# Optimization experiments

Hardware: AMD Instinct MI355X
Metric: run time of the kernel (lower is better)

Reference implementation:

```python
import jax, jax.numpy as jnp
import numpy as np

EPS = 1e-6


def setup_inputs() -> dict:
    key = jax.random.key(0)
    k1, _ = jax.random.split(key)
    L, D = 128, 262144
    slots = jax.random.normal(k1, (L, D), dtype=jnp.float32)
    temperature = jnp.ones((), dtype=jnp.float32)  # temperature = 1.0
    return {"slots": slots, "temperature": temperature, "length": L}


def reference(slots, temperature, length):
    # slots: [L, D]; pairwise cosine similarity (torch: x.y / max(|x||y|, eps))
    L = length
    norms = jnp.sqrt(jnp.sum(slots * slots, axis=1))                # [L]
    gram = jnp.einsum('id,jd->ij', slots, slots)                    # [L, L]
    sim = gram / jnp.maximum(norms[:, None] * norms[None, :], EPS)  # [L, L]
    logits = sim / temperature
    E = jnp.exp(logits)                                             # [L, L]
    # denominator for pair (i, j): sum_{k != j} exp(sim(i,k)/T)  (k=i included)
    denom = jnp.sum(E, axis=1, keepdims=True) - E                   # [L, L]
    log_ratio = logits - jnp.log(denom)                             # log(num/den)
    idx = jnp.arange(L)
    penalty = jnp.abs(idx[:, None] - idx[None, :]).astype(slots.dtype)  # |i-j|
    upper = (idx[:, None] < idx[None, :]).astype(slots.dtype)           # i < j
    total = jnp.sum(-log_ratio * penalty * upper)
    # original divides by i*j/2 with final loop values i=j=length-1
    total = total / ((L - 1) * (L - 1) / 2.0)
    return total
```

## Files before the change

### kernel.cpp

```cpp
#include <hip/hip_runtime.h>
#include <hip/hip_bf16.h>

typedef __attribute__((ext_vector_type(8))) short bf16x8;
typedef __attribute__((ext_vector_type(4))) float f32x4;

constexpr int L  = 128;
constexpr int BK = 128;
constexpr int LDS_PITCH = BK * 2;
constexpr int GRID = 512;

__device__ inline bf16x8 ld_frag(const char* lds, int row, int kk, int lane) {
    int byteoff = row * LDS_PITCH + (kk + 8 * (lane >> 4)) * 2;
    byteoff ^= (row & 7) << 4;
    return *reinterpret_cast<const bf16x8*>(lds + byteoff);
}

__global__ __launch_bounds__(256, 2)
void gram_kernel(const float* __restrict__ slots, float* __restrict__ partial,
                 int D, int nChunks, int G) {
    __shared__ __align__(16) char lds[2][L * LDS_PITCH];
    const int t    = threadIdx.x;
    const int wave = t >> 6;
    const int lane = t & 63;

    f32x4 acc[2][8];
#pragma unroll
    for (int r = 0; r < 2; ++r)
#pragma unroll
        for (int c = 0; c < 8; ++c) acc[r][c] = (f32x4)0.f;

    float4 ld[16];

    auto issue = [&](int chunk) {
        const size_t c0 = (size_t)chunk * BK;
#pragma unroll
        for (int q = 0; q < 16; ++q) {
            int idx  = t + 256 * q;
            int row  = idx >> 5;
            int col4 = idx & 31;
            ld[q] = *reinterpret_cast<const float4*>(
                slots + (size_t)row * D + c0 + (size_t)col4 * 4);
        }
    };
    auto commit = [&](int buf) {
#pragma unroll
        for (int q = 0; q < 16; ++q) {
            int idx  = t + 256 * q;
            int row  = idx >> 5;
            int col4 = idx & 31;
            const unsigned int* f = reinterpret_cast<const unsigned int*>(&ld[q]);
            uint2 p;
            p.x = __builtin_amdgcn_perm(f[1], f[0], 0x07060302u);
            p.y = __builtin_amdgcn_perm(f[3], f[2], 0x07060302u);
            int byteoff = row * LDS_PITCH + col4 * 8;
            byteoff ^= (row & 7) << 4;
            *reinterpret_cast<uint2*>(&lds[buf][0] + byteoff) = p;
        }
    };

    issue(blockIdx.x);
    commit(0);
    __syncthreads();

    int k = 0;
    for (int c = blockIdx.x; c < nChunks; c += G, ++k) {
        const int nxt = c + G;
        if (nxt < nChunks) issue(nxt);
        const int cur = k & 1;

#pragma unroll
        for (int kk = 0; kk < BK; kk += 32) {
            bf16x8 a0 = ld_frag(&lds[cur][0], wave * 32 +      (lane & 15), kk, lane);
            bf16x8 a1 = ld_frag(&lds[cur][0], wave * 32 + 16 + (lane & 15), kk, lane);
#pragma unroll
            for (int cc = 0; cc < 8; ++cc) {
                bf16x8 b = ld_frag(&lds[cur][0], cc * 16 + (lane & 15), kk, lane);
                acc[0][cc] = __builtin_amdgcn_mfma_f32_16x16x32_bf16(a0, b, acc[0][cc], 0, 0, 0);
                acc[1][cc] = __builtin_amdgcn_mfma_f32_16x16x32_bf16(a1, b, acc[1][cc], 0, 0, 0);
            }
        }

        if (nxt < nChunks) commit(cur ^ 1);
        __syncthreads();
    }

    float* pb = partial + (size_t)blockIdx.x * (L * L);
#pragma unroll
    for (int r = 0; r < 2; ++r)
#pragma unroll
        for (int c = 0; c < 8; ++c)
            *reinterpret_cast<float4*>(pb + (r * 8 + c) * 1024 + t * 4) =
                *reinterpret_cast<float4*>(&acc[r][c]);
}

__global__ void zero_kernel(float* __restrict__ p, int n) {
    int i = blockIdx.x * 256 + threadIdx.x;
    if (i < n) p[i] = 0.f;
}

__global__ void reduce_kernel(const float* __restrict__ partial, float* __restrict__ gram,
                              int G, int span) {
    const int id = blockIdx.x * 256 + threadIdx.x;
    const int b0 = blockIdx.y * span;
    const int b1 = (b0 + span < G) ? b0 + span : G;

    float4 sum = make_float4(0.f, 0.f, 0.f, 0.f);
    for (int b = b0; b < b1; ++b) {
        const float4 v = *reinterpret_cast<const float4*>(
            partial + (size_t)b * (L * L) + (size_t)id * 4);
        sum.x += v.x; sum.y += v.y; sum.z += v.z; sum.w += v.w;
    }
    const int tt   = id & 255;
    const int slot = id >> 8;
    const int wave = tt >> 6, lane = tt & 63;
    const int r = slot >> 3, c = slot & 7;
    const int growb = wave * 32 + r * 16 + ((lane >> 4) << 2);
    const int gcol  = c * 16 + (lane & 15);
    atomicAdd(&gram[(growb + 0) * L + gcol], sum.x);
    atomicAdd(&gram[(growb + 1) * L + gcol], sum.y);
    atomicAdd(&gram[(growb + 2) * L + gcol], sum.z);
    atomicAdd(&gram[(growb + 3) * L + gcol], sum.w);
}

__global__ __launch_bounds__(1024, 1)
void finalize_kernel(const float* __restrict__ gram,
                     const float* __restrict__ temperature,
                     float* __restrict__ out) {
    __shared__ float g[L * L];
    __shared__ float norms[L];
    __shared__ float wsum[16];
    const int t = threadIdx.x;

#pragma unroll
    for (int q = 0; q < 4; ++q) {
        int i = t + 1024 * q;
        *reinterpret_cast<float4*>(&g[i * 4]) =
            *reinterpret_cast<const float4*>(&gram[i * 4]);
    }
    __syncthreads();
    if (t < L) norms[t] = sqrtf(g[t * L + t]);
    __syncthreads();

    const float invT = 1.0f / temperature[0];
    const int r = t >> 3;
    const int q = t & 7;
    const float ni = norms[r];

    float ps = 0.f;
    for (int j = q; j < L; j += 8) {
        float sim = g[r * L + j] / fmaxf(ni * norms[j], 1e-6f);
        ps += __expf(sim * invT);
    }
    ps += __shfl_xor(ps, 1);
    ps += __shfl_xor(ps, 2);
    ps += __shfl_xor(ps, 4);
    const float rowsum = ps;

    float tot = 0.f;
    for (int j = q; j < L; j += 8) {
        if (j > r) {
            float logit = (g[r * L + j] / fmaxf(ni * norms[j], 1e-6f)) * invT;
            float e = __expf(logit);
            tot += -(logit - __logf(rowsum - e)) * (float)(j - r);
        }
    }
#pragma unroll
    for (int s = 1; s < 64; s <<= 1) tot += __shfl_xor(tot, s);
    if ((t & 63) == 0) wsum[t >> 6] = tot;
    __syncthreads();
    if (t == 0) {
        float s = 0.f;
        for (int w = 0; w < 16; ++w) s += wsum[w];
        out[0] = s / ((float)(L - 1) * (float)(L - 1) * 0.5f);
    }
}

extern "C" void kernel_launch(void* const* d_in, const int* in_sizes, int n_in,
                              void* d_out, int out_size, void* d_ws, size_t ws_size,
                              hipStream_t stream) {
    const float* slots       = (const float*)d_in[0];
    const float* temperature = (const float*)d_in[1];
    float* out  = (float*)d_out;

    const int D = in_sizes[0] / L;
    const int nChunks = D / BK;
    int G = GRID;
    if (G > nChunks) G = nChunks;

    float* partial = (float*)d_ws;
    float* gram    = (float*)d_ws + (size_t)G * L * L;

    zero_kernel<<<(L * L + 255) / 256, 256, 0, stream>>>(gram, L * L);
    gram_kernel<<<G, 256, 0, stream>>>(slots, partial, D, nChunks, G);

    const int NY = 8;
    dim3 rgrid(16, NY);
    reduce_kernel<<<rgrid, 256, 0, stream>>>(partial, gram, G, (G + NY - 1) / NY);

    finalize_kernel<<<1, 1024, 0, stream>>>(gram, temperature, out);
}
```

Baseline: 59.99 us.

## Store bf16 transposed partials and fuse reduce with finalize via last-block ticket

The gram kernel now packs its fp32 accumulators to bf16 and writes them in a transposed layout (slot-major, block-minor), which halves partial traffic and makes the per-element reduction contiguous. The zero, atomic reduce and single-block finalize kernels are replaced by one kernel: 256 blocks each reduce 8 slots with wave shuffles and write gram directly, then the last block to take an atomic ticket computes the loss. This removes two launches and the atomics. The cost is bf16 rounding of the partial sums, which may hurt accuracy, and a finalize step that now runs on 256 threads reading global memory instead of 1024 threads reading LDS.

```diff
diff --git a/kernel.cpp b/kernel.cpp
--- a/kernel.cpp
+++ b/kernel.cpp
@@ -16,12 +16,14 @@
 }
 
 __global__ __launch_bounds__(256, 2)
-void gram_kernel(const float* __restrict__ slots, float* __restrict__ partial,
-                 int D, int nChunks, int G) {
-    __shared__ __align__(16) char lds[2][L * LDS_PITCH];
+void gram_kernel(const float* __restrict__ slots, uint4* __restrict__ pT,
+                 unsigned* __restrict__ counter, int D, int nChunks, int G) {
+    __shared__ __align__(16) char smem[2][L * LDS_PITCH];
     const int t    = threadIdx.x;
     const int wave = t >> 6;
     const int lane = t & 63;
+
+    if (blockIdx.x == 0 && t == 0) *counter = 0;
 
     f32x4 acc[2][8];
 #pragma unroll
@@ -54,7 +56,7 @@
             p.y = __builtin_amdgcn_perm(f[3], f[2], 0x07060302u);
             int byteoff = row * LDS_PITCH + col4 * 8;
             byteoff ^= (row & 7) << 4;
-            *reinterpret_cast<uint2*>(&lds[buf][0] + byteoff) = p;
+            *reinterpret_cast<uint2*>(&smem[buf][0] + byteoff) = p;
         }
     };
 
@@ -70,11 +72,11 @@
 
 #pragma unroll
         for (int kk = 0; kk < BK; kk += 32) {
-            bf16x8 a0 = ld_frag(&lds[cur][0], wave * 32 +      (lane & 15), kk, lane);
-            bf16x8 a1 = ld_frag(&lds[cur][0], wave * 32 + 16 + (lane & 15), kk, lane);
+            bf16x8 a0 = ld_frag(&smem[cur][0], wave * 32 +      (lane & 15), kk, lane);
+            bf16x8 a1 = ld_frag(&smem[cur][0], wave * 32 + 16 + (lane & 15), kk, lane);
 #pragma unroll
             for (int cc = 0; cc < 8; ++cc) {
-                bf16x8 b = ld_frag(&lds[cur][0], cc * 16 + (lane & 15), kk, lane);
+                bf16x8 b = ld_frag(&smem[cur][0], cc * 16 + (lane & 15), kk, lane);
                 acc[0][cc] = __builtin_amdgcn_mfma_f32_16x16x32_bf16(a0, b, acc[0][cc], 0, 0, 0);
                 acc[1][cc] = __builtin_amdgcn_mfma_f32_16x16x32_bf16(a1, b, acc[1][cc], 0, 0, 0);
             }
@@ -84,95 +86,108 @@
         __syncthreads();
     }
 
-    float* pb = partial + (size_t)blockIdx.x * (L * L);
 #pragma unroll
     for (int r = 0; r < 2; ++r)
 #pragma unroll
-        for (int c = 0; c < 8; ++c)
-            *reinterpret_cast<float4*>(pb + (r * 8 + c) * 1024 + t * 4) =
-                *reinterpret_cast<float4*>(&acc[r][c]);
-}
-
-__global__ void zero_kernel(float* __restrict__ p, int n) {
-    int i = blockIdx.x * 256 + threadIdx.x;
-    if (i < n) p[i] = 0.f;
-}
-
-__global__ void reduce_kernel(const float* __restrict__ partial, float* __restrict__ gram,
-                              int G, int span) {
-    const int id = blockIdx.x * 256 + threadIdx.x;
-    const int b0 = blockIdx.y * span;
-    const int b1 = (b0 + span < G) ? b0 + span : G;
-
-    float4 sum = make_float4(0.f, 0.f, 0.f, 0.f);
-    for (int b = b0; b < b1; ++b) {
-        const float4 v = *reinterpret_cast<const float4*>(
-            partial + (size_t)b * (L * L) + (size_t)id * 4);
-        sum.x += v.x; sum.y += v.y; sum.z += v.z; sum.w += v.w;
-    }
-    const int tt   = id & 255;
-    const int slot = id >> 8;
-    const int wave = tt >> 6, lane = tt & 63;
-    const int r = slot >> 3, c = slot & 7;
-    const int growb = wave * 32 + r * 16 + ((lane >> 4) << 2);
-    const int gcol  = c * 16 + (lane & 15);
-    atomicAdd(&gram[(growb + 0) * L + gcol], sum.x);
-    atomicAdd(&gram[(growb + 1) * L + gcol], sum.y);
-    atomicAdd(&gram[(growb + 2) * L + gcol], sum.z);
-    atomicAdd(&gram[(growb + 3) * L + gcol], sum.w);
-}
-
-__global__ __launch_bounds__(1024, 1)
-void finalize_kernel(const float* __restrict__ gram,
-                     const float* __restrict__ temperature,
-                     float* __restrict__ out) {
-    __shared__ float g[L * L];
+        for (int c2 = 0; c2 < 4; ++c2) {
+            const unsigned* e = reinterpret_cast<const unsigned*>(&acc[r][2 * c2]);
+            const unsigned* o = reinterpret_cast<const unsigned*>(&acc[r][2 * c2 + 1]);
+            uint4 u;
+            u.x = __builtin_amdgcn_perm(e[1], e[0], 0x07060302u);
+            u.y = __builtin_amdgcn_perm(e[3], e[2], 0x07060302u);
+            u.z = __builtin_amdgcn_perm(o[1], o[0], 0x07060302u);
+            u.w = __builtin_amdgcn_perm(o[3], o[2], 0x07060302u);
+            int s = (r * 4 + c2) * 256 + t;
+            pT[(size_t)s * G + blockIdx.x] = u;
+        }
+}
+
+__device__ inline float blo(unsigned w) { unsigned v = w << 16;          return __builtin_bit_cast(float, v); }
+__device__ inline float bhi(unsigned w) { unsigned v = w & 0xffff0000u;  return __builtin_bit_cast(float, v); }
+
+__global__ __launch_bounds__(256)
+void reduce_finalize(const uint4* __restrict__ pT, float* __restrict__ gram,
+                     unsigned* __restrict__ counter,
+                     const float* __restrict__ temperature, float* __restrict__ out,
+                     int G) {
     __shared__ float norms[L];
-    __shared__ float wsum[16];
-    const int t = threadIdx.x;
-
-#pragma unroll
-    for (int q = 0; q < 4; ++q) {
-        int i = t + 1024 * q;
-        *reinterpret_cast<float4*>(&g[i * 4]) =
-            *reinterpret_cast<const float4*>(&gram[i * 4]);
-    }
-    __syncthreads();
-    if (t < L) norms[t] = sqrtf(g[t * L + t]);
+    __shared__ float wred[4];
+    __shared__ unsigned ticket_s;
+    const int t  = threadIdx.x;
+    const int g  = t >> 5;
+    const int ln = t & 31;
+    const int s  = blockIdx.x * 8 + g;
+
+    float a8[8];
+#pragma unroll
+    for (int j = 0; j < 8; ++j) a8[j] = 0.f;
+
+    const uint4* base = pT + (size_t)s * G;
+#pragma unroll 16
+    for (int p = ln; p < G; p += 32) {
+        uint4 u = base[p];
+        a8[0] += blo(u.x); a8[1] += bhi(u.x);
+        a8[2] += blo(u.y); a8[3] += bhi(u.y);
+        a8[4] += blo(u.z); a8[5] += bhi(u.z);
+        a8[6] += blo(u.w); a8[7] += bhi(u.w);
+    }
+#pragma unroll
+    for (int m = 1; m <= 16; m <<= 1)
+#pragma unroll
+        for (int j = 0; j < 8; ++j) a8[j] += __shfl_xor(a8[j], m);
+
+    if (ln == 0) {
+        const int rc = s >> 8, tenc = s & 255;
+        const int r = rc >> 2, c2 = rc & 3;
+        const int wv = tenc >> 6, le = tenc & 63;
+        const int growb = wv * 32 + r * 16 + ((le >> 4) << 2);
+        const int gE = (2 * c2) * 16 + (le & 15);
+#pragma unroll
+        for (int j = 0; j < 4; ++j) {
+            gram[(growb + j) * L + gE]      = a8[j];
+            gram[(growb + j) * L + gE + 16] = a8[4 + j];
+        }
+    }
+
+    __syncthreads();
+    if (t == 0) {
+        __threadfence();
+        ticket_s = atomicAdd(counter, 1u);
+    }
+    __syncthreads();
+    if (ticket_s != (unsigned)(gridDim.x - 1)) return;
+    __threadfence();
+
+    if (t < L) norms[t] = sqrtf(gram[t * L + t]);
     __syncthreads();
 
     const float invT = 1.0f / temperature[0];
-    const int r = t >> 3;
-    const int q = t & 7;
+    const int r = t >> 1;
+    const int q = t & 1;
     const float ni = norms[r];
 
     float ps = 0.f;
-    for (int j = q; j < L; j += 8) {
-        float sim = g[r * L + j] / fmaxf(ni * norms[j], 1e-6f);
+    for (int j = q; j < L; j += 2) {
+        float sim = gram[r * L + j] / fmaxf(ni * norms[j], 1e-6f);
         ps += __expf(sim * invT);
     }
     ps += __shfl_xor(ps, 1);
-    ps += __shfl_xor(ps, 2);
-    ps += __shfl_xor(ps, 4);
     const float rowsum = ps;
 
     float tot = 0.f;
-    for (int j = q; j < L; j += 8) {
+    for (int j = q; j < L; j += 2) {
         if (j > r) {
-            float logit = (g[r * L + j] / fmaxf(ni * norms[j], 1e-6f)) * invT;
-            float e = __expf(logit);
-            tot += -(logit - __logf(rowsum - e)) * (float)(j - r);
-        }
-    }
-#pragma unroll
-    for (int s = 1; s < 64; s <<= 1) tot += __shfl_xor(tot, s);
-    if ((t & 63) == 0) wsum[t >> 6] = tot;
-    __syncthreads();
-    if (t == 0) {
-        float s = 0.f;
-        for (int w = 0; w < 16; ++w) s += wsum[w];
-        out[0] = s / ((float)(L - 1) * (float)(L - 1) * 0.5f);
-    }
+            float logit = (gram[r * L + j] / fmaxf(ni * norms[j], 1e-6f)) * invT;
+            tot += -(logit - __logf(rowsum - __expf(logit))) * (float)(j - r);
+        }
+    }
+#pragma unroll
+    for (int m = 1; m < 64; m <<= 1) tot += __shfl_xor(tot, m);
+    if ((t & 63) == 0) wred[t >> 6] = tot;
+    __syncthreads();
+    if (t == 0)
+        out[0] = (wred[0] + wred[1] + wred[2] + wred[3]) /
+                 ((float)(L - 1) * (float)(L - 1) * 0.5f);
 }
 
 extern "C" void kernel_launch(void* const* d_in, const int* in_sizes, int n_in,
@@ -187,15 +202,10 @@
     int G = GRID;
     if (G > nChunks) G = nChunks;
 
-    float* partial = (float*)d_ws;
-    float* gram    = (float*)d_ws + (size_t)G * L * L;
-
-    zero_kernel<<<(L * L + 255) / 256, 256, 0, stream>>>(gram, L * L);
-    gram_kernel<<<G, 256, 0, stream>>>(slots, partial, D, nChunks, G);
-
-    const int NY = 8;
-    dim3 rgrid(16, NY);
-    reduce_kernel<<<rgrid, 256, 0, stream>>>(partial, gram, G, (G + NY - 1) / NY);
-
-    finalize_kernel<<<1, 1024, 0, stream>>>(gram, temperature, out);
-}
+    uint4*    pT      = (uint4*)d_ws;
+    float*    gram    = (float*)((char*)d_ws + (size_t)2048 * G * 16);
+    unsigned* counter = (unsigned*)((char*)gram + (size_t)L * L * 4);
+
+    gram_kernel<<<G, 256, 0, stream>>>(slots, pT, counter, D, nChunks, G);
+    reduce_finalize<<<256, 256, 0, stream>>>(pT, gram, counter, temperature, out, G);
+}
```

Result: slower. 74.25 us (+23.8%).
